# Performance work log

Measured on AMD Instinct MI355X. Metric: run time of the kernel, lower is better.

Reference implementation:

```python
import jax, jax.numpy as jnp
import numpy as np

ALPHA = 0.5
SIGMA = 0.5
EPS = 1e-7

def setup_inputs() -> dict:
    key = jax.random.key(0)
    k1, k2, k3, k4 = jax.random.split(key, 4)
    n, T = 8192, 256
    return {
        "hazards": jax.random.normal(k1, (n, T), dtype=jnp.float32),
        "duration": jax.random.randint(k2, (n,), 0, T, dtype=jnp.int32),
        "event": jax.random.randint(k3, (n,), 0, 2, dtype=jnp.int32),
        "label": jax.random.randint(k4, (n,), 0, T, dtype=jnp.int32),
    }

def _deephit_loss(hazards, duration, event, label):
    dur = duration.reshape(-1)
    ev = event.reshape(-1)
    lab = label.reshape(-1)
    evf = ev.astype(hazards.dtype)

    # pair_rank_mat: R_ij = 1{D_i=1 and (T_i < T_j or (T_i == T_j and D_j = 0))}
    rank_mat = ((ev[:, None] != 0)
                & ((dur[:, None] < dur[None, :])
                   | ((dur[:, None] == dur[None, :]) & (ev[None, :] == 0)))
                ).astype(hazards.dtype)  # [n, n]

    # nll_pmf (pad_col adds a zero column -> T+1 bins)
    phi = jnp.pad(hazards, ((0, 0), (0, 1)))            # [n, T+1]
    gamma = jnp.max(phi, axis=1)                         # [n]
    cumsum = jnp.cumsum(jnp.exp(phi - gamma[:, None]), axis=1)  # [n, T+1]
    sum_ = cumsum[:, -1]
    phi_at = jnp.take_along_axis(phi, lab[:, None], axis=1)[:, 0]
    cum_at = jnp.take_along_axis(cumsum, lab[:, None], axis=1)[:, 0]
    part1 = (phi_at - gamma) * evf
    part2 = -jnp.log(jnp.maximum(sum_, 0.0) + EPS)
    part3 = jnp.log(jnp.maximum(sum_ - cum_at, 0.0) + EPS) * (1.0 - evf)
    nll = jnp.mean(-(part1 + part2 + part3))

    # rank_loss_deephit_single
    pmf = jax.nn.softmax(phi, axis=1)                    # [n, T+1]
    cdf = jnp.cumsum(pmf, axis=1)                        # [n, T+1]
    y = jax.nn.one_hot(lab, phi.shape[1], dtype=pmf.dtype)  # [n, T+1]
    r = cdf @ y.T                                        # r_ij = F_i(T_j), [n, n]
    diag_r = jnp.diagonal(r)                             # F_j(T_j)
    r = (diag_r[None, :] - r).T                          # r_ij = F_i(T_i) - F_j(T_i)
    rank_loss = jnp.mean(rank_mat * jnp.exp(-r / SIGMA))

    return ALPHA * nll + (1.0 - ALPHA) * rank_loss

def reference(hazards, duration, event, label):
    return _deephit_loss(hazards, duration, event, label)
```

## Files before the change

### kernel.cpp

```cpp
#include <hip/hip_runtime.h>

#define TBINS 256
#define EPS_F 1e-7f
#define INV_SIGMA 2.0f
#define RPB 16

__global__ void zero_acc_kernel(float* acc) {
    if (threadIdx.x < 2) acc[threadIdx.x] = 0.0f;
}

__global__ __launch_bounds__(1024) void row_kernel(
    const float* __restrict__ hz, const int* __restrict__ dur,
    const int* __restrict__ ev,  const int* __restrict__ lab,
    float* __restrict__ WT, float* __restrict__ rowA,
    float* __restrict__ acc, int n)
{
    __shared__ float trs[RPB][260];
    __shared__ float nllred[RPB];

    const int wid  = threadIdx.x >> 6;
    const int lane = threadIdx.x & 63;
    const int row  = blockIdx.x * RPB + wid;
    const bool active = row < n;
    const int rrow = active ? row : 0;

    const float4* hv = (const float4*)(hz + (size_t)rrow * TBINS);
    float4 v = hv[lane];

    float m = fmaxf(fmaxf(v.x, v.y), fmaxf(v.z, v.w));
    #pragma unroll
    for (int off = 32; off; off >>= 1) m = fmaxf(m, __shfl_xor(m, off));
    const float gamma = fmaxf(m, 0.0f);

    const float e0 = expf(v.x - gamma);
    const float e1 = expf(v.y - gamma);
    const float e2 = expf(v.z - gamma);
    const float e3 = expf(v.w - gamma);
    const float local = e0 + e1 + e2 + e3;

    float pre = local;
    #pragma unroll
    for (int off = 1; off < 64; off <<= 1) {
        float t = __shfl_up(pre, off);
        if (lane >= off) pre += t;
    }
    const float excl  = pre - local;
    const float total = __shfl(pre, 63);
    const float sum_  = total + expf(-gamma);

    const float c0 = excl + e0;
    const float c1 = c0 + e1;
    const float c2 = c1 + e2;
    const float c3 = c2 + e3;

    const int L = lab[rrow];
    const int d = dur[rrow];
    const int e = ev[rrow];
    (void)d;

    const int sel = L & 3;
    float csel = (sel == 0) ? c0 : (sel == 1) ? c1 : (sel == 2) ? c2 : c3;
    const float cum_at = __shfl(csel, L >> 2);

    const float inv = 1.0f / sum_;

    float4 w;
    w.x = expf(c0 * inv * INV_SIGMA);
    w.y = expf(c1 * inv * INV_SIGMA);
    w.z = expf(c2 * inv * INV_SIGMA);
    w.w = expf(c3 * inv * INV_SIGMA);
    *(float4*)&trs[wid][4 * lane] = w;

    float nll_i = 0.0f;
    if (lane == 0) {
        if (active) {
            const float phi_at = hz[(size_t)row * TBINS + L];
            const float evf = (float)e;
            const float part1 = (phi_at - gamma) * evf;
            const float part2 = -logf(fmaxf(sum_, 0.0f) + EPS_F);
            const float part3 = logf(fmaxf(sum_ - cum_at, 0.0f) + EPS_F) * (1.0f - evf);
            nll_i = -(part1 + part2 + part3);
            const float a = cum_at * inv;
            rowA[row] = e ? expf(-a * INV_SIGMA) : 0.0f;
        }
        nllred[wid] = nll_i;
    }
    __syncthreads();

    if (threadIdx.x == 0) {
        float s = 0.0f;
        #pragma unroll
        for (int k = 0; k < RPB; ++k) s += nllred[k];
        atomicAdd(&acc[0], s);
    }

    const int t  = threadIdx.x >> 2;
    const int q  = threadIdx.x & 3;
    const int i0 = blockIdx.x * RPB + 4 * q;
    if (i0 + 3 < n) {
        float4 o;
        o.x = trs[4 * q + 0][t];
        o.y = trs[4 * q + 1][t];
        o.z = trs[4 * q + 2][t];
        o.w = trs[4 * q + 3][t];
        *(float4*)&WT[(size_t)t * n + i0] = o;
    }
}

__global__ __launch_bounds__(1024) void agg_kernel(
    const float* __restrict__ WT, const int* __restrict__ dur,
    const int* __restrict__ ev, float* __restrict__ B, int n)
{
    __shared__ float binsG[TBINS];
    __shared__ float binsG0[TBINS];
    __shared__ float scan[TBINS];

    const int t   = blockIdx.x;
    const int tid = threadIdx.x;

    if (tid < TBINS) { binsG[tid] = 0.0f; binsG0[tid] = 0.0f; }
    __syncthreads();

    const float* w = WT + (size_t)t * n;
    for (int i = tid; i < n; i += 1024) {
        const float v = w[i];
        const int d = dur[i];
        atomicAdd(&binsG[d], v);
        if (ev[i] == 0) atomicAdd(&binsG0[d], v);
    }
    __syncthreads();

    if (tid < TBINS) scan[tid] = binsG[tid];
    __syncthreads();
    for (int off = 1; off < TBINS; off <<= 1) {
        float add = 0.0f;
        if (tid < TBINS && tid >= off) add = scan[tid - off];
        __syncthreads();
        if (tid < TBINS) scan[tid] += add;
        __syncthreads();
    }
    if (tid < TBINS) {
        const float total = scan[TBINS - 1];
        const float suffix = total - scan[tid];
        B[t * TBINS + tid] = suffix + binsG0[tid];
    }
}

__global__ __launch_bounds__(256) void rank_kernel(
    const int* __restrict__ dur, const int* __restrict__ ev,
    const int* __restrict__ lab, const float* __restrict__ rowA,
    const float* __restrict__ B, float* __restrict__ acc, int n)
{
    const int i = blockIdx.x * blockDim.x + threadIdx.x;
    float val = 0.0f;
    if (i < n && ev[i]) {
        val = rowA[i] * B[lab[i] * TBINS + dur[i]];
    }
    #pragma unroll
    for (int off = 32; off; off >>= 1) val += __shfl_xor(val, off);
    __shared__ float s[4];
    if ((threadIdx.x & 63) == 0) s[threadIdx.x >> 6] = val;
    __syncthreads();
    if (threadIdx.x == 0) atomicAdd(&acc[1], s[0] + s[1] + s[2] + s[3]);
}

__global__ void final_kernel(const float* __restrict__ acc, float* __restrict__ out, int n)
{
    const double nll = (double)acc[0] / (double)n;
    const double rl  = (double)acc[1] / ((double)n * (double)n);
    out[0] = (float)(0.5 * nll + 0.5 * rl);
}

extern "C" void kernel_launch(void* const* d_in, const int* in_sizes, int n_in,
                              void* d_out, int out_size, void* d_ws, size_t ws_size,
                              hipStream_t stream) {
    const float* hz  = (const float*)d_in[0];
    const int*   dur = (const int*)d_in[1];
    const int*   ev  = (const int*)d_in[2];
    const int*   lab = (const int*)d_in[3];
    float* out = (float*)d_out;

    const int n = in_sizes[1];

    float* WT   = (float*)d_ws;
    float* B    = WT + (size_t)TBINS * n;
    float* rowA = B + TBINS * TBINS;
    float* acc  = rowA + n;

    zero_acc_kernel<<<1, 64, 0, stream>>>(acc);
    row_kernel<<<(n + RPB - 1) / RPB, 1024, 0, stream>>>(hz, dur, ev, lab, WT, rowA, acc, n);
    agg_kernel<<<TBINS, 1024, 0, stream>>>(WT, dur, ev, B, n);
    rank_kernel<<<(n + 255) / 256, 256, 0, stream>>>(dur, ev, lab, rowA, B, acc, n);
    final_kernel<<<1, 1, 0, stream>>>(acc, out, n);
}
```

Before: 95.62 us.

## Fuse row, aggregation and rank kernels into one cooperative kernel with grid syncs

Replaces the five separate kernel launches with one cooperative kernel of 256 blocks. Grid-wide syncs separate the row pass, the per-bin aggregation and the rank reduction, and each block now handles 32 rows. Per-block partial sums replace the global atomics, and a final reduction in block 0 removes the zero and final kernels. This cuts launch overhead and inter-kernel gaps, but it hardwires NBLK=256 (so n must equal 8192 for full row coverage) and grid.sync adds cost on 256 blocks.

Result: slower. 192.8 us (+101.6%).

```diff
diff --git a/kernel.cpp b/kernel.cpp
--- a/kernel.cpp
+++ b/kernel.cpp
@@ -1,174 +1,173 @@
 #include <hip/hip_runtime.h>
+#include <hip/hip_cooperative_groups.h>
+
+namespace cg = cooperative_groups;
 
 #define TBINS 256
+#define NBLK  256
+#define NTHR  1024
+#define RPB   32
 #define EPS_F 1e-7f
 #define INV_SIGMA 2.0f
-#define RPB 16
 
-__global__ void zero_acc_kernel(float* acc) {
-    if (threadIdx.x < 2) acc[threadIdx.x] = 0.0f;
-}
-
-__global__ __launch_bounds__(1024) void row_kernel(
+__global__ __launch_bounds__(NTHR) void fused_kernel(
     const float* __restrict__ hz, const int* __restrict__ dur,
     const int* __restrict__ ev,  const int* __restrict__ lab,
-    float* __restrict__ WT, float* __restrict__ rowA,
-    float* __restrict__ acc, int n)
+    float* __restrict__ WT, float* __restrict__ B,
+    float* __restrict__ nllpart, float* __restrict__ rankpart,
+    float* __restrict__ out, int n)
 {
+    cg::grid_group grid = cg::this_grid();
+
     __shared__ float trs[RPB][260];
     __shared__ float nllred[RPB];
+    __shared__ float rA[RPB];
+    __shared__ float binsG[TBINS];
+    __shared__ float binsG0[TBINS];
+    __shared__ float scan[TBINS];
+    __shared__ float fs[16], fr[16];
 
-    const int wid  = threadIdx.x >> 6;
-    const int lane = threadIdx.x & 63;
-    const int row  = blockIdx.x * RPB + wid;
-    const bool active = row < n;
-    const int rrow = active ? row : 0;
+    const int blk  = blockIdx.x;
+    const int tid  = threadIdx.x;
+    const int wid  = tid >> 6;
+    const int lane = tid & 63;
 
-    const float4* hv = (const float4*)(hz + (size_t)rrow * TBINS);
-    float4 v = hv[lane];
+    #pragma unroll
+    for (int r = 0; r < 2; ++r) {
+        const int lrow = wid * 2 + r;
+        const int row  = blk * RPB + lrow;
+        const bool act = row < n;
+        const int rrow = act ? row : 0;
 
-    float m = fmaxf(fmaxf(v.x, v.y), fmaxf(v.z, v.w));
-    #pragma unroll
-    for (int off = 32; off; off >>= 1) m = fmaxf(m, __shfl_xor(m, off));
-    const float gamma = fmaxf(m, 0.0f);
+        const float4 v = ((const float4*)(hz + (size_t)rrow * TBINS))[lane];
 
-    const float e0 = expf(v.x - gamma);
-    const float e1 = expf(v.y - gamma);
-    const float e2 = expf(v.z - gamma);
-    const float e3 = expf(v.w - gamma);
-    const float local = e0 + e1 + e2 + e3;
+        float m = fmaxf(fmaxf(v.x, v.y), fmaxf(v.z, v.w));
+        #pragma unroll
+        for (int off = 32; off; off >>= 1) m = fmaxf(m, __shfl_xor(m, off));
+        const float gamma = fmaxf(m, 0.0f);
 
-    float pre = local;
-    #pragma unroll
-    for (int off = 1; off < 64; off <<= 1) {
-        float t = __shfl_up(pre, off);
-        if (lane >= off) pre += t;
-    }
-    const float excl  = pre - local;
-    const float total = __shfl(pre, 63);
-    const float sum_  = total + expf(-gamma);
+        const float e0 = expf(v.x - gamma), e1 = expf(v.y - gamma);
+        const float e2 = expf(v.z - gamma), e3 = expf(v.w - gamma);
+        const float local = e0 + e1 + e2 + e3;
 
-    const float c0 = excl + e0;
-    const float c1 = c0 + e1;
-    const float c2 = c1 + e2;
-    const float c3 = c2 + e3;
+        float pre = local;
+        #pragma unroll
+        for (int off = 1; off < 64; off <<= 1) {
+            float t = __shfl_up(pre, off);
+            if (lane >= off) pre += t;
+        }
+        const float excl  = pre - local;
+        const float total = __shfl(pre, 63);
+        const float sum_  = total + expf(-gamma);
+        const float c0 = excl + e0, c1 = c0 + e1, c2 = c1 + e2, c3 = c2 + e3;
 
-    const int L = lab[rrow];
-    const int d = dur[rrow];
-    const int e = ev[rrow];
-    (void)d;
+        const int L = lab[rrow];
+        const int e = ev[rrow];
+        const int sel = L & 3;
+        float csel = (sel == 0) ? c0 : (sel == 1) ? c1 : (sel == 2) ? c2 : c3;
+        const float cum_at = __shfl(csel, L >> 2);
+        const float inv = 1.0f / sum_;
 
-    const int sel = L & 3;
-    float csel = (sel == 0) ? c0 : (sel == 1) ? c1 : (sel == 2) ? c2 : c3;
-    const float cum_at = __shfl(csel, L >> 2);
+        float4 w;
+        w.x = expf(c0 * inv * INV_SIGMA);
+        w.y = expf(c1 * inv * INV_SIGMA);
+        w.z = expf(c2 * inv * INV_SIGMA);
+        w.w = expf(c3 * inv * INV_SIGMA);
+        *(float4*)&trs[lrow][4 * lane] = w;
 
-    const float inv = 1.0f / sum_;
-
-    float4 w;
-    w.x = expf(c0 * inv * INV_SIGMA);
-    w.y = expf(c1 * inv * INV_SIGMA);
-    w.z = expf(c2 * inv * INV_SIGMA);
-    w.w = expf(c3 * inv * INV_SIGMA);
-    *(float4*)&trs[wid][4 * lane] = w;
-
-    float nll_i = 0.0f;
-    if (lane == 0) {
-        if (active) {
-            const float phi_at = hz[(size_t)row * TBINS + L];
-            const float evf = (float)e;
-            const float part1 = (phi_at - gamma) * evf;
-            const float part2 = -logf(fmaxf(sum_, 0.0f) + EPS_F);
-            const float part3 = logf(fmaxf(sum_ - cum_at, 0.0f) + EPS_F) * (1.0f - evf);
-            nll_i = -(part1 + part2 + part3);
-            const float a = cum_at * inv;
-            rowA[row] = e ? expf(-a * INV_SIGMA) : 0.0f;
+        if (lane == 0) {
+            float nll_i = 0.f, a_i = 0.f;
+            if (act) {
+                const float phi_at = hz[(size_t)row * TBINS + L];
+                const float evf = (float)e;
+                const float p1 = (phi_at - gamma) * evf;
+                const float p2 = -logf(fmaxf(sum_, 0.f) + EPS_F);
+                const float p3 = logf(fmaxf(sum_ - cum_at, 0.f) + EPS_F) * (1.f - evf);
+                nll_i = -(p1 + p2 + p3);
+                a_i = e ? expf(-(cum_at * inv) * INV_SIGMA) : 0.f;
+            }
+            nllred[lrow] = nll_i;
+            rA[lrow]     = a_i;
         }
-        nllred[wid] = nll_i;
     }
     __syncthreads();
 
-    if (threadIdx.x == 0) {
-        float s = 0.0f;
+    #pragma unroll
+    for (int k = 0; k < 2; ++k) {
+        const int t = (tid >> 3) + 128 * k;
+        const int j = tid & 7;
+        float4 o;
+        o.x = trs[4 * j + 0][t];
+        o.y = trs[4 * j + 1][t];
+        o.z = trs[4 * j + 2][t];
+        o.w = trs[4 * j + 3][t];
+        const int i0 = blk * RPB + 4 * j;
+        if (i0 + 3 < n) *(float4*)&WT[(size_t)t * n + i0] = o;
+    }
+    if (tid == 0) {
+        float s = 0.f;
         #pragma unroll
         for (int k = 0; k < RPB; ++k) s += nllred[k];
-        atomicAdd(&acc[0], s);
+        nllpart[blk] = s;
     }
+    grid.sync();
 
-    const int t  = threadIdx.x >> 2;
-    const int q  = threadIdx.x & 3;
-    const int i0 = blockIdx.x * RPB + 4 * q;
-    if (i0 + 3 < n) {
-        float4 o;
-        o.x = trs[4 * q + 0][t];
-        o.y = trs[4 * q + 1][t];
-        o.z = trs[4 * q + 2][t];
-        o.w = trs[4 * q + 3][t];
-        *(float4*)&WT[(size_t)t * n + i0] = o;
-    }
-}
-
-__global__ __launch_bounds__(1024) void agg_kernel(
-    const float* __restrict__ WT, const int* __restrict__ dur,
-    const int* __restrict__ ev, float* __restrict__ B, int n)
-{
-    __shared__ float binsG[TBINS];
-    __shared__ float binsG0[TBINS];
-    __shared__ float scan[TBINS];
-
-    const int t   = blockIdx.x;
-    const int tid = threadIdx.x;
-
-    if (tid < TBINS) { binsG[tid] = 0.0f; binsG0[tid] = 0.0f; }
+    if (tid < TBINS) { binsG[tid] = 0.f; binsG0[tid] = 0.f; }
     __syncthreads();
-
-    const float* w = WT + (size_t)t * n;
-    for (int i = tid; i < n; i += 1024) {
-        const float v = w[i];
-        const int d = dur[i];
-        atomicAdd(&binsG[d], v);
-        if (ev[i] == 0) atomicAdd(&binsG0[d], v);
+    {
+        const float* wrow = WT + (size_t)blk * n;
+        for (int i = tid; i < n; i += NTHR) {
+            const float v = wrow[i];
+            const int d = dur[i];
+            atomicAdd(&binsG[d], v);
+            if (ev[i] == 0) atomicAdd(&binsG0[d], v);
+        }
     }
     __syncthreads();
-
     if (tid < TBINS) scan[tid] = binsG[tid];
     __syncthreads();
     for (int off = 1; off < TBINS; off <<= 1) {
-        float add = 0.0f;
+        float add = 0.f;
         if (tid < TBINS && tid >= off) add = scan[tid - off];
         __syncthreads();
         if (tid < TBINS) scan[tid] += add;
         __syncthreads();
     }
-    if (tid < TBINS) {
-        const float total = scan[TBINS - 1];
-        const float suffix = total - scan[tid];
-        B[t * TBINS + tid] = suffix + binsG0[tid];
+    if (tid < TBINS)
+        B[blk * TBINS + tid] = (scan[TBINS - 1] - scan[tid]) + binsG0[tid];
+    grid.sync();
+
+    float val = 0.f;
+    if (tid < RPB) {
+        const int row = blk * RPB + tid;
+        if (row < n && ev[row]) val = rA[tid] * B[lab[row] * TBINS + dur[row]];
     }
-}
+    if (wid == 0) {
+        #pragma unroll
+        for (int off = 32; off; off >>= 1) val += __shfl_xor(val, off);
+        if (tid == 0) rankpart[blk] = val;
+    }
+    grid.sync();
 
-__global__ __launch_bounds__(256) void rank_kernel(
-    const int* __restrict__ dur, const int* __restrict__ ev,
-    const int* __restrict__ lab, const float* __restrict__ rowA,
-    const float* __restrict__ B, float* __restrict__ acc, int n)
-{
-    const int i = blockIdx.x * blockDim.x + threadIdx.x;
-    float val = 0.0f;
-    if (i < n && ev[i]) {
-        val = rowA[i] * B[lab[i] * TBINS + dur[i]];
+    if (blk == 0) {
+        float s  = (tid < NBLK) ? nllpart[tid]  : 0.f;
+        float r2 = (tid < NBLK) ? rankpart[tid] : 0.f;
+        #pragma unroll
+        for (int off = 32; off; off >>= 1) {
+            s  += __shfl_xor(s, off);
+            r2 += __shfl_xor(r2, off);
+        }
+        if (lane == 0) { fs[wid] = s; fr[wid] = r2; }
+        __syncthreads();
+        if (tid == 0) {
+            float S = 0.f, R = 0.f;
+            #pragma unroll
+            for (int k = 0; k < 16; ++k) { S += fs[k]; R += fr[k]; }
+            const double nll = (double)S / (double)n;
+            const double rl  = (double)R / ((double)n * (double)n);
+            out[0] = (float)(0.5 * nll + 0.5 * rl);
+        }
     }
-    #pragma unroll
-    for (int off = 32; off; off >>= 1) val += __shfl_xor(val, off);
-    __shared__ float s[4];
-    if ((threadIdx.x & 63) == 0) s[threadIdx.x >> 6] = val;
-    __syncthreads();
-    if (threadIdx.x == 0) atomicAdd(&acc[1], s[0] + s[1] + s[2] + s[3]);
-}
-
-__global__ void final_kernel(const float* __restrict__ acc, float* __restrict__ out, int n)
-{
-    const double nll = (double)acc[0] / (double)n;
-    const double rl  = (double)acc[1] / ((double)n * (double)n);
-    out[0] = (float)(0.5 * nll + 0.5 * rl);
 }
 
 extern "C" void kernel_launch(void* const* d_in, const int* in_sizes, int n_in,
@@ -180,16 +179,16 @@
     const int*   lab = (const int*)d_in[3];
     float* out = (float*)d_out;
 
-    const int n = in_sizes[1];
+    int n = in_sizes[1];
 
-    float* WT   = (float*)d_ws;
-    float* B    = WT + (size_t)TBINS * n;
-    float* rowA = B + TBINS * TBINS;
-    float* acc  = rowA + n;
+    float* WT       = (float*)d_ws;
+    float* B        = WT + (size_t)TBINS * n;
+    float* nllpart  = B + TBINS * TBINS;
+    float* rankpart = nllpart + NBLK;
 
-    zero_acc_kernel<<<1, 64, 0, stream>>>(acc);
-    row_kernel<<<(n + RPB - 1) / RPB, 1024, 0, stream>>>(hz, dur, ev, lab, WT, rowA, acc, n);
-    agg_kernel<<<TBINS, 1024, 0, stream>>>(WT, dur, ev, B, n);
-    rank_kernel<<<(n + 255) / 256, 256, 0, stream>>>(dur, ev, lab, rowA, B, acc, n);
-    final_kernel<<<1, 1, 0, stream>>>(acc, out, n);
+    void* args[] = { (void*)&hz, (void*)&dur, (void*)&ev, (void*)&lab,
+                     (void*)&WT, (void*)&B, (void*)&nllpart, (void*)&rankpart,
+                     (void*)&out, (void*)&n };
+    hipLaunchCooperativeKernel((const void*)fused_kernel,
+                               dim3(NBLK), dim3(NTHR), args, 0, stream);
 }
```
